# Kernel tuning notes

Measured on AMD Instinct MI355X. Metric: run time of the kernel, lower is better.

Reference implementation:

```python
import jax, jax.numpy as jnp
import numpy as np

B, S, D = 4, 2048, 1024

def setup_inputs() -> dict:
    key = jax.random.key(0)
    ks = jax.random.split(key, 7)
    sc = 1.0 / np.sqrt(D)
    return {
        "x": jax.random.normal(ks[0], (B, S, D), dtype=jnp.float32),
        "Wq": jax.random.normal(ks[1], (D, D), dtype=jnp.float32) * sc,
        "bq": jax.random.normal(ks[2], (D,), dtype=jnp.float32) * 0.01,
        "Wk": jax.random.normal(ks[3], (D, D), dtype=jnp.float32) * sc,
        "bk": jax.random.normal(ks[4], (D,), dtype=jnp.float32) * 0.01,
        "Wv": jax.random.normal(ks[5], (D, D), dtype=jnp.float32) * sc,
        "bv": jax.random.normal(ks[6], (D,), dtype=jnp.float32) * 0.01,
    }

def reference(x, Wq, bq, Wk, bk, Wv, bv):
    # q, k, v: [B, S, D] projections (torch Linear: x @ W^T + b; here W stored as [in, out])
    q = jnp.einsum("bsd,df->bsf", x, Wq) + bq
    k = jnp.einsum("bsd,df->bsf", x, Wk) + bk
    v = jnp.einsum("bsd,df->bsf", x, Wv) + bv
    dim = x.shape[-1]
    # scores: [B, S, S], scaled by sqrt(full d_model) as in the source
    scores = jnp.einsum("bqd,bkd->bqk", q, k) / jnp.sqrt(jnp.float32(dim)).astype(x.dtype)
    attn = jax.nn.softmax(scores, axis=-1)
    return jnp.einsum("bqk,bkd->bqd", attn, v)
```

## Files before the change

### kernel.cpp

```cpp
#include <hip/hip_runtime.h>
#include <hip/hip_bf16.h>

typedef __attribute__((ext_vector_type(8))) short bf16x8;
typedef __attribute__((ext_vector_type(4))) float f32x4;
typedef unsigned short u16;

__device__ __forceinline__ u16 f2bf(float f) {
  unsigned int u = __builtin_bit_cast(unsigned int, f);
  u += 0x7fffu + ((u >> 16) & 1u);
  return (u16)(u >> 16);
}
__device__ __forceinline__ float bf2f(unsigned int h) {
  unsigned int u = h << 16;
  return __builtin_bit_cast(float, u);
}

__device__ __forceinline__ void gload_lds16(const void* g, void* l) {
  __builtin_amdgcn_global_load_lds(
      (const __attribute__((address_space(1))) void*)g,
      (__attribute__((address_space(3))) void*)l, 16, 0, 0);
}

#define BAR() __builtin_amdgcn_s_barrier()
#define LGKM0() asm volatile("s_waitcnt lgkmcnt(0)" ::: "memory")
#define LGKM8() asm volatile("s_waitcnt lgkmcnt(8)" ::: "memory")
#define VMC(N) asm volatile("s_waitcnt vmcnt(%0)" ::"n"(N) : "memory")

template <int EPI>
__global__ __launch_bounds__(512, 2) void gemm8x(
    const u16* __restrict__ Abase, const u16* __restrict__ Btbase,
    const float* __restrict__ bq, const float* __restrict__ bk,
    const float* __restrict__ bv, void* __restrict__ out0,
    void* __restrict__ out1, void* __restrict__ out2, int Kd, int ldc,
    long long sAz, long long sBz, long long sCz) {
  constexpr int HSZ = 16384;
  constexpr int BUFSZ = 4 * HSZ;
  __shared__ char lds[2 * BUFSZ];

  const int tid = threadIdx.x;
  const int w = tid >> 6, l = tid & 63;
  const int wr = w >> 2, wc = w & 3;
  const int lq = l >> 4, lr = l & 15;
  const int bm = blockIdx.y * 256, bn = blockIdx.x * 256;
  const int z = blockIdx.z;
  const u16* A = Abase + (size_t)z * sAz;
  const u16* Bt = Btbase + (size_t)z * sBz;
  const int NTk = Kd >> 6, NI = NTk >> 1;

  const int kbp = ((tid & 7) ^ ((tid >> 3) & 7)) * 8;
  const int drow = tid >> 3;
  const u16* gA[2][2];
  const u16* gB[2][2];
#pragma unroll
  for (int h = 0; h < 2; ++h)
#pragma unroll
    for (int u = 0; u < 2; ++u) {
      gA[h][u] = A + (size_t)(bm + h * 128 + u * 64 + drow) * Kd + kbp;
      gB[h][u] = Bt + (size_t)(bn + h * 128 + u * 64 + drow) * Kd + kbp;
    }

  auto stageA = [&](int buf, int h, int kt) {
    char* d = lds + buf * BUFSZ + h * HSZ + tid * 16;
    gload_lds16(gA[h][0] + kt * 64, d);
    gload_lds16(gA[h][1] + kt * 64, d + 8192);
  };
  auto stageB = [&](int buf, int h, int kt) {
    char* d = lds + buf * BUFSZ + (2 + h) * HSZ + tid * 16;
    gload_lds16(gB[h][0] + kt * 64, d);
    gload_lds16(gB[h][1] + kt * 64, d + 8192);
  };

  const int rA = wr * 64 + lr;
  const int rB = wc * 32 + lr;
  int aoff[2], boff[2];
#pragma unroll
  for (int kh = 0; kh < 2; ++kh) {
    aoff[kh] = rA * 128 + (((kh * 4 + lq) ^ (rA & 7)) << 4);
    boff[kh] = rB * 128 + (((kh * 4 + lq) ^ (rB & 7)) << 4);
  }

  f32x4 acc[2][4][2][2] = {};
  bf16x8 a[2][4];
  bf16x8 bb[2][2][2];

#define RD_A(BUF, MQ)                                                       \
  {                                                                         \
    const char* p_ = lds + (BUF)*BUFSZ + (MQ)*HSZ;                          \
    _Pragma("unroll") for (int kh = 0; kh < 2; ++kh)                        \
        _Pragma("unroll") for (int mf = 0; mf < 4; ++mf) a[kh][mf] =        \
            *(const bf16x8*)(p_ + aoff[kh] + mf * 2048);                    \
  }
#define RD_B(BUF, NQ)                                                       \
  {                                                                         \
    const char* p_ = lds + (BUF)*BUFSZ + (2 + (NQ)) * HSZ;                  \
    _Pragma("unroll") for (int kh = 0; kh < 2; ++kh)                        \
        _Pragma("unroll") for (int nf = 0; nf < 2; ++nf) bb[NQ][kh][nf] =   \
            *(const bf16x8*)(p_ + boff[kh] + nf * 2048);                    \
  }
#define MMAQ(MQ, NQ)                                                          \
  {                                                                           \
    __builtin_amdgcn_s_setprio(1);                                            \
    _Pragma("unroll") for (int kh = 0; kh < 2; ++kh)                          \
        _Pragma("unroll") for (int mf = 0; mf < 4; ++mf)                      \
            _Pragma("unroll") for (int nf = 0; nf < 2; ++nf) acc[MQ][mf][NQ]  \
                [nf] = __builtin_amdgcn_mfma_f32_16x16x32_bf16(               \
                    a[kh][mf], bb[NQ][kh][nf], acc[MQ][mf][NQ][nf], 0, 0, 0); \
    __builtin_amdgcn_s_setprio(0);                                            \
  }

  stageA(0, 0, 0);
  stageB(0, 0, 0);
  stageB(0, 1, 0);
  stageA(0, 1, 0);
  stageA(1, 0, 1);
  stageB(1, 0, 1);
  stageB(1, 1, 1);
  VMC(6);
  BAR();

  for (int i = 0; i < NI; ++i) {
    const int kt1 = 2 * i + 1, ktn0 = 2 * i + 2, ktn1 = 2 * i + 3;
    const bool s0 = ktn0 < NTk, s1 = ktn1 < NTk;
    RD_A(0, 0);
    RD_B(0, 0);
    stageA(1, 1, kt1);
    LGKM8();
    BAR();
    LGKM0();
    MMAQ(0, 0);
    BAR();
    RD_B(0, 1);
    if (s0) stageA(0, 0, ktn0);
    BAR();
    LGKM0();
    MMAQ(0, 1);
    BAR();
    RD_A(0, 1);
    if (s0) stageB(0, 0, ktn0);
    BAR();
    LGKM0();
    MMAQ(1, 1);
    BAR();
    if (s0) stageB(0, 1, ktn0);
    BAR();
    MMAQ(1, 0);
    if (i + 1 < NI) VMC(6); else VMC(0);
    BAR();
    RD_A(1, 0);
    RD_B(1, 0);
    if (s0) stageA(0, 1, ktn0);
    LGKM8();
    BAR();
    LGKM0();
    MMAQ(0, 0);
    BAR();
    RD_B(1, 1);
    if (s1) stageA(1, 0, ktn1);
    BAR();
    LGKM0();
    MMAQ(0, 1);
    BAR();
    RD_A(1, 1);
    if (s1) stageB(1, 0, ktn1);
    BAR();
    LGKM0();
    MMAQ(1, 1);
    BAR();
    if (s1) stageB(1, 1, ktn1);
    BAR();
    MMAQ(1, 0);
    VMC(6);
    BAR();
  }

  if constexpr (EPI == 0) {
    const int mat = bn >> 10;
    const float sc = (mat == 0) ? 0.03125f : 1.0f;
    const float* bias = (mat == 0) ? bq : (mat == 1 ? bk : bv);
    u16* Q = (u16*)out0;
    u16* K = (u16*)out1;
    u16* V = (u16*)out2;
#pragma unroll
    for (int nq = 0; nq < 2; ++nq)
#pragma unroll
      for (int nf = 0; nf < 2; ++nf) {
        const int oc = ((bn + wc * 32 + nq * 128 + nf * 16 + lr) & 1023);
        const float bv2 = bias[oc];
#pragma unroll
        for (int mq = 0; mq < 2; ++mq)
#pragma unroll
          for (int mf = 0; mf < 4; ++mf) {
            const int row = bm + wr * 64 + mq * 128 + mf * 16 + lq * 4;
            if (mat < 2) {
              u16* dst = (mat == 0) ? Q : K;
#pragma unroll
              for (int e = 0; e < 4; ++e)
                dst[(size_t)(row + e) * 1024 + oc] =
                    f2bf((acc[mq][mf][nq][nf][e] + bv2) * sc);
            } else {
              const int bz = row >> 11, sdx = row & 2047;
              ushort4 pk;
              pk.x = f2bf(acc[mq][mf][nq][nf][0] + bv2);
              pk.y = f2bf(acc[mq][mf][nq][nf][1] + bv2);
              pk.z = f2bf(acc[mq][mf][nq][nf][2] + bv2);
              pk.w = f2bf(acc[mq][mf][nq][nf][3] + bv2);
              *(ushort4*)&V[((size_t)bz * 1024 + oc) * 2048 + sdx] = pk;
            }
          }
      }
  } else {
    u16* C = (u16*)out0 + (size_t)z * sCz;
#pragma unroll
    for (int nq = 0; nq < 2; ++nq)
#pragma unroll
      for (int nf = 0; nf < 2; ++nf) {
        const int col = bn + wc * 32 + nq * 128 + nf * 16 + lr;
#pragma unroll
        for (int mq = 0; mq < 2; ++mq)
#pragma unroll
          for (int mf = 0; mf < 4; ++mf) {
            const int row = bm + wr * 64 + mq * 128 + mf * 16 + lq * 4;
#pragma unroll
            for (int e = 0; e < 4; ++e)
              C[(size_t)(row + e) * ldc + col] = f2bf(acc[mq][mf][nq][nf][e]);
          }
      }
  }
#undef RD_A
#undef RD_B
#undef MMAQ
}

__global__ __launch_bounds__(512, 2) void gemm2v(
    const u16* __restrict__ Abase, const u16* __restrict__ Btbase,
    float* __restrict__ outp, int Kd, int ldc, long long sAz, long long sBz,
    long long sCz) {
  constexpr int ASZ = 16384;
  constexpr int BSZ = 32768;
  constexpr int BBASE = 2 * ASZ;
  __shared__ char lds[2 * ASZ + 3 * BSZ];

  const int tid = threadIdx.x;
  const int w = tid >> 6, l = tid & 63;
  const int wr = w >> 2, wc = w & 3;
  const int lq = l >> 4, lr = l & 15;
  const int bm = blockIdx.y * 128, bn = blockIdx.x * 256;
  const int z = blockIdx.z;
  const u16* A = Abase + (size_t)z * sAz;
  const u16* Bt = Btbase + (size_t)z * sBz;
  const int NT = Kd >> 6;

  const int kbp = ((tid & 7) ^ ((tid >> 3) & 7)) * 8;
  const int drow = tid >> 3;
  const u16* gA[2];
  const u16* gB[4];
#pragma unroll
  for (int u = 0; u < 2; ++u)
    gA[u] = A + (size_t)(bm + u * 64 + drow) * Kd + kbp;
#pragma unroll
  for (int u = 0; u < 4; ++u)
    gB[u] = Bt + (size_t)(bn + u * 64 + drow) * Kd + kbp;

  auto stageA = [&](int kt) {
    char* d = lds + (kt & 1) * ASZ + tid * 16;
#pragma unroll
    for (int u = 0; u < 2; ++u) gload_lds16(gA[u] + kt * 64, d + u * 8192);
  };
  auto stageB = [&](int kt) {
    char* d = lds + BBASE + (kt % 3) * BSZ + tid * 16;
#pragma unroll
    for (int u = 0; u < 4; ++u) gload_lds16(gB[u] + kt * 64, d + u * 8192);
  };

  const int rA = wr * 64 + lr;
  const int rB0 = wc * 64 + lr;
  int aoff[2];
#pragma unroll
  for (int kh = 0; kh < 2; ++kh)
    aoff[kh] = rA * 128 + (((kh * 4 + lq) ^ (rA & 7)) << 4);

  f32x4 acc[4][2][2] = {};
  bf16x8 a[2][4], b[2][2];

  auto rdA = [&](int kt) {
    const char* p = lds + (kt & 1) * ASZ;
#pragma unroll
    for (int kh = 0; kh < 2; ++kh)
#pragma unroll
      for (int mf = 0; mf < 4; ++mf)
        a[kh][mf] = *(const bf16x8*)(p + aoff[kh] + mf * 2048);
  };
  auto rdB = [&](int kt, int nh) {
    const char* p = lds + BBASE + (kt % 3) * BSZ;
    const int rB = rB0 + nh * 32;
#pragma unroll
    for (int kh = 0; kh < 2; ++kh) {
      const int o = rB * 128 + (((kh * 4 + lq) ^ (rB & 7)) << 4);
#pragma unroll
      for (int nf = 0; nf < 2; ++nf)
        b[kh][nf] = *(const bf16x8*)(p + o + nf * 2048);
    }
  };
  auto mma = [&](int nh) {
    __builtin_amdgcn_s_setprio(1);
#pragma unroll
    for (int kh = 0; kh < 2; ++kh)
#pragma unroll
      for (int mf = 0; mf < 4; ++mf)
#pragma unroll
        for (int nf = 0; nf < 2; ++nf)
          acc[mf][nh][nf] = __builtin_amdgcn_mfma_f32_16x16x32_bf16(
              a[kh][mf], b[kh][nf], acc[mf][nh][nf], 0, 0, 0);
    __builtin_amdgcn_s_setprio(0);
  };

  stageB(0);
  stageA(0);
  stageB(1);
  stageA(1);
  VMC(6);
  BAR();

  for (int t = 0; t < NT; ++t) {
    rdA(t);
    rdB(t, 0);
    if (t + 2 < NT) stageB(t + 2);
    LGKM8();
    BAR();
    LGKM0();
    mma(0);
    BAR();
    rdB(t, 1);
    if (t + 2 < NT) stageA(t + 2);
    BAR();
    LGKM0();
    mma(1);
    if (t + 3 <= NT) VMC(6); else VMC(0);
    BAR();
  }

  float* C = outp + (size_t)z * sCz;
#pragma unroll
  for (int nh = 0; nh < 2; ++nh)
#pragma unroll
    for (int nf = 0; nf < 2; ++nf) {
      const int col = bn + wc * 64 + nh * 32 + nf * 16 + lr;
#pragma unroll
      for (int mf = 0; mf < 4; ++mf) {
        const int row = bm + wr * 64 + mf * 16 + lq * 4;
#pragma unroll
        for (int e = 0; e < 4; ++e)
          C[(size_t)(row + e) * ldc + col] = acc[mf][nh][nf][e];
      }
    }
}

__global__ __launch_bounds__(256) void cvt_x(const float* __restrict__ in,
                                             u16* __restrict__ out) {
  const int i = blockIdx.x * 256 + threadIdx.x;
  const float4 v = ((const float4*)in)[i];
  ushort4 o;
  o.x = f2bf(v.x);
  o.y = f2bf(v.y);
  o.z = f2bf(v.z);
  o.w = f2bf(v.w);
  ((ushort4*)out)[i] = o;
}

__global__ void cvt_wt(const float* __restrict__ Wq,
                       const float* __restrict__ Wk,
                       const float* __restrict__ Wv, u16* __restrict__ Wt) {
  __shared__ float s[32][33];
  const float* W = blockIdx.z == 0 ? Wq : (blockIdx.z == 1 ? Wk : Wv);
  u16* O = Wt + (size_t)blockIdx.z * 1048576;
  const int k0 = blockIdx.y * 32, n0 = blockIdx.x * 32;
  s[threadIdx.y][threadIdx.x] =
      W[(size_t)(k0 + threadIdx.y) * 1024 + n0 + threadIdx.x];
  __syncthreads();
  O[(size_t)(n0 + threadIdx.y) * 1024 + k0 + threadIdx.x] =
      f2bf(s[threadIdx.x][threadIdx.y]);
}

__global__ __launch_bounds__(256) void softmax_rows(u16* __restrict__ SP) {
  const size_t base = ((size_t)blockIdx.y * 2048 + blockIdx.x) * 2048;
  u16* p = SP + base;
  const int t = threadIdx.x;
  __shared__ float red[4];

  uint4 u = ((const uint4*)p)[t];
  unsigned int uu[4] = {u.x, u.y, u.z, u.w};
  float f[8];
#pragma unroll
  for (int j = 0; j < 4; ++j) {
    f[2 * j] = bf2f(uu[j] & 0xffffu);
    f[2 * j + 1] = __builtin_bit_cast(float, uu[j] & 0xffff0000u);
  }
  float mx = f[0];
#pragma unroll
  for (int i = 1; i < 8; ++i) mx = fmaxf(mx, f[i]);
#pragma unroll
  for (int o = 32; o; o >>= 1) mx = fmaxf(mx, __shfl_xor(mx, o, 64));
  if ((t & 63) == 0) red[t >> 6] = mx;
  __syncthreads();
  mx = fmaxf(fmaxf(red[0], red[1]), fmaxf(red[2], red[3]));
  __syncthreads();

  float e[8];
  float sum = 0.f;
#pragma unroll
  for (int i = 0; i < 8; ++i) {
    e[i] = __expf(f[i] - mx);
    sum += e[i];
  }
#pragma unroll
  for (int o = 32; o; o >>= 1) sum += __shfl_xor(sum, o, 64);
  if ((t & 63) == 0) red[t >> 6] = sum;
  __syncthreads();
  sum = red[0] + red[1] + red[2] + red[3];
  const float inv = 1.0f / sum;

  uint4 ov;
  unsigned int w0[4];
#pragma unroll
  for (int j = 0; j < 4; ++j) {
    unsigned int lo = f2bf(e[2 * j] * inv);
    unsigned int hi = f2bf(e[2 * j + 1] * inv);
    w0[j] = lo | (hi << 16);
  }
  ov.x = w0[0];
  ov.y = w0[1];
  ov.z = w0[2];
  ov.w = w0[3];
  ((uint4*)p)[t] = ov;
}

extern "C" void kernel_launch(void* const* d_in, const int* in_sizes, int n_in,
                              void* d_out, int out_size, void* d_ws,
                              size_t ws_size, hipStream_t stream) {
  const float* x = (const float*)d_in[0];
  const float* Wq = (const float*)d_in[1];
  const float* bq = (const float*)d_in[2];
  const float* Wk = (const float*)d_in[3];
  const float* bk = (const float*)d_in[4];
  const float* Wv = (const float*)d_in[5];
  const float* bv = (const float*)d_in[6];
  float* out = (float*)d_out;
  char* ws = (char*)d_ws;

  u16* xb = (u16*)ws;
  u16* Wt = (u16*)(ws + 16777216);
  u16* Qb = (u16*)(ws + 23068672);
  u16* Kb = Qb + 8388608;
  u16* Vt = Kb + 8388608;
  u16* SP = Vt + 8388608;

  cvt_x<<<8192, 256, 0, stream>>>(x, xb);
  cvt_wt<<<dim3(32, 32, 3), dim3(32, 32), 0, stream>>>(Wq, Wk, Wv, Wt);

  gemm8x<0><<<dim3(12, 32, 1), 512, 0, stream>>>(
      xb, Wt, bq, bk, bv, Qb, Kb, Vt, 1024, 0, 0, 0, 0);

  gemm8x<2><<<dim3(8, 8, 4), 512, 0, stream>>>(
      Qb, Kb, nullptr, nullptr, nullptr, SP, nullptr, nullptr, 1024, 2048,
      2097152LL, 2097152LL, 4194304LL);

  softmax_rows<<<dim3(2048, 4), 256, 0, stream>>>(SP);

  gemm2v<<<dim3(4, 16, 4), 512, 0, stream>>>(
      SP, Vt, out, 2048, 1024, 4194304LL, 2097152LL, 2097152LL);
}
```

Measured before the change: 181.1 us.

## Restructure GEMM main loops with fewer barriers and split A register sets

Rewrites the software pipelines of both GEMM kernels. The 256x256 kernel now iterates one k-tile per loop step. It keeps separate even and odd A fragment register sets, reads both B quarters up front, and removes explicit lgkmcnt waits and several barriers. The gemm2v kernel reads all B fragments at once, splits the MMA by k-half instead of n-half, and drops a barrier per iteration. The aim is to cut synchronisation overhead and let LDS reads overlap MFMA, at the cost of more register pressure and reliance on compiler-inserted waits for correctness.

```diff
diff --git a/kernel.cpp b/kernel.cpp
--- a/kernel.cpp
+++ b/kernel.cpp
@@ -22,8 +22,6 @@
 }
 
 #define BAR() __builtin_amdgcn_s_barrier()
-#define LGKM0() asm volatile("s_waitcnt lgkmcnt(0)" ::: "memory")
-#define LGKM8() asm volatile("s_waitcnt lgkmcnt(8)" ::: "memory")
 #define VMC(N) asm volatile("s_waitcnt vmcnt(%0)" ::"n"(N) : "memory")
 
 template <int EPI>
@@ -45,7 +43,7 @@
   const int z = blockIdx.z;
   const u16* A = Abase + (size_t)z * sAz;
   const u16* Bt = Btbase + (size_t)z * sBz;
-  const int NTk = Kd >> 6, NI = NTk >> 1;
+  const int NTk = Kd >> 6;
 
   const int kbp = ((tid & 7) ^ ((tid >> 3) & 7)) * 8;
   const int drow = tid >> 3;
@@ -80,31 +78,39 @@
   }
 
   f32x4 acc[2][4][2][2] = {};
-  bf16x8 a[2][4];
+  bf16x8 aE[2][4], aO[2][4];
   bf16x8 bb[2][2][2];
 
-#define RD_A(BUF, MQ)                                                       \
-  {                                                                         \
-    const char* p_ = lds + (BUF)*BUFSZ + (MQ)*HSZ;                          \
-    _Pragma("unroll") for (int kh = 0; kh < 2; ++kh)                        \
-        _Pragma("unroll") for (int mf = 0; mf < 4; ++mf) a[kh][mf] =        \
-            *(const bf16x8*)(p_ + aoff[kh] + mf * 2048);                    \
-  }
-#define RD_B(BUF, NQ)                                                       \
-  {                                                                         \
-    const char* p_ = lds + (BUF)*BUFSZ + (2 + (NQ)) * HSZ;                  \
-    _Pragma("unroll") for (int kh = 0; kh < 2; ++kh)                        \
-        _Pragma("unroll") for (int nf = 0; nf < 2; ++nf) bb[NQ][kh][nf] =   \
-            *(const bf16x8*)(p_ + boff[kh] + nf * 2048);                    \
-  }
-#define MMAQ(MQ, NQ)                                                          \
+#define RD_AE(BUF)                                                        \
+  {                                                                       \
+    const char* p_ = lds + (BUF)*BUFSZ;                                   \
+    _Pragma("unroll") for (int kh = 0; kh < 2; ++kh)                      \
+        _Pragma("unroll") for (int mf = 0; mf < 4; ++mf) aE[kh][mf] =     \
+            *(const bf16x8*)(p_ + aoff[kh] + mf * 2048);                  \
+  }
+#define RD_AO(BUF)                                                        \
+  {                                                                       \
+    const char* p_ = lds + (BUF)*BUFSZ + HSZ;                             \
+    _Pragma("unroll") for (int kh = 0; kh < 2; ++kh)                      \
+        _Pragma("unroll") for (int mf = 0; mf < 4; ++mf) aO[kh][mf] =     \
+            *(const bf16x8*)(p_ + aoff[kh] + mf * 2048);                  \
+  }
+#define RD_B(BUF, NQ)                                                     \
+  {                                                                       \
+    const char* p_ = lds + (BUF)*BUFSZ + (2 + (NQ)) * HSZ;                \
+    _Pragma("unroll") for (int kh = 0; kh < 2; ++kh)                      \
+        _Pragma("unroll") for (int nf = 0; nf < 2; ++nf) bb[NQ][kh][nf] = \
+            *(const bf16x8*)(p_ + boff[kh] + nf * 2048);                  \
+  }
+#define MMAQ(MQ, NQ, ASET)                                                    \
   {                                                                           \
     __builtin_amdgcn_s_setprio(1);                                            \
     _Pragma("unroll") for (int kh = 0; kh < 2; ++kh)                          \
         _Pragma("unroll") for (int mf = 0; mf < 4; ++mf)                      \
             _Pragma("unroll") for (int nf = 0; nf < 2; ++nf) acc[MQ][mf][NQ]  \
                 [nf] = __builtin_amdgcn_mfma_f32_16x16x32_bf16(               \
-                    a[kh][mf], bb[NQ][kh][nf], acc[MQ][mf][NQ][nf], 0, 0, 0); \
+                    ASET[kh][mf], bb[NQ][kh][nf], acc[MQ][mf][NQ][nf], 0, 0,  \
+                    0);                                                       \
     __builtin_amdgcn_s_setprio(0);                                            \
   }
 
@@ -118,59 +124,29 @@
   VMC(6);
   BAR();
 
-  for (int i = 0; i < NI; ++i) {
-    const int kt1 = 2 * i + 1, ktn0 = 2 * i + 2, ktn1 = 2 * i + 3;
-    const bool s0 = ktn0 < NTk, s1 = ktn1 < NTk;
-    RD_A(0, 0);
-    RD_B(0, 0);
-    stageA(1, 1, kt1);
-    LGKM8();
-    BAR();
-    LGKM0();
-    MMAQ(0, 0);
-    BAR();
-    RD_B(0, 1);
-    if (s0) stageA(0, 0, ktn0);
-    BAR();
-    LGKM0();
-    MMAQ(0, 1);
-    BAR();
-    RD_A(0, 1);
-    if (s0) stageB(0, 0, ktn0);
-    BAR();
-    LGKM0();
-    MMAQ(1, 1);
-    BAR();
-    if (s0) stageB(0, 1, ktn0);
-    BAR();
-    MMAQ(1, 0);
-    if (i + 1 < NI) VMC(6); else VMC(0);
-    BAR();
-    RD_A(1, 0);
-    RD_B(1, 0);
-    if (s0) stageA(0, 1, ktn0);
-    LGKM8();
-    BAR();
-    LGKM0();
-    MMAQ(0, 0);
-    BAR();
-    RD_B(1, 1);
-    if (s1) stageA(1, 0, ktn1);
-    BAR();
-    LGKM0();
-    MMAQ(0, 1);
-    BAR();
-    RD_A(1, 1);
-    if (s1) stageB(1, 0, ktn1);
-    BAR();
-    LGKM0();
-    MMAQ(1, 1);
-    BAR();
-    if (s1) stageB(1, 1, ktn1);
-    BAR();
-    MMAQ(1, 0);
-    VMC(6);
-    BAR();
+  for (int t = 0; t < NTk; ++t) {
+    const int buf = t & 1;
+    const bool deep = (t + 2 < NTk);
+    if (deep) VMC(6); else VMC(0);
+    RD_AE(buf);
+    RD_B(buf, 0);
+    RD_B(buf, 1);
+    if (t + 1 < NTk) stageA(buf ^ 1, 1, t + 1);
+    BAR();
+    MMAQ(0, 0, aE);
+    if (deep) VMC(6); else VMC(0);
+    RD_AO(buf);
+    if (deep) stageA(buf, 0, t + 2);
+    BAR();
+    MMAQ(0, 1, aE);
+    if (deep) VMC(6); else VMC(0);
+    if (deep) stageB(buf, 0, t + 2);
+    BAR();
+    MMAQ(1, 1, aO);
+    if (deep) VMC(6); else VMC(0);
+    if (deep) stageB(buf, 1, t + 2);
+    BAR();
+    MMAQ(1, 0, aO);
   }
 
   if constexpr (EPI == 0) {
@@ -226,7 +202,8 @@
           }
       }
   }
-#undef RD_A
+#undef RD_AE
+#undef RD_AO
 #undef RD_B
 #undef MMAQ
 }
@@ -280,7 +257,8 @@
     aoff[kh] = rA * 128 + (((kh * 4 + lq) ^ (rA & 7)) << 4);
 
   f32x4 acc[4][2][2] = {};
-  bf16x8 a[2][4], b[2][2];
+  bf16x8 a[2][4];
+  bf16x8 bb[2][2][2];
 
   auto rdA = [&](int kt) {
     const char* p = lds + (kt & 1) * ASZ;
@@ -290,27 +268,30 @@
       for (int mf = 0; mf < 4; ++mf)
         a[kh][mf] = *(const bf16x8*)(p + aoff[kh] + mf * 2048);
   };
-  auto rdB = [&](int kt, int nh) {
+  auto rdB = [&](int kt) {
     const char* p = lds + BBASE + (kt % 3) * BSZ;
-    const int rB = rB0 + nh * 32;
-#pragma unroll
-    for (int kh = 0; kh < 2; ++kh) {
-      const int o = rB * 128 + (((kh * 4 + lq) ^ (rB & 7)) << 4);
-#pragma unroll
-      for (int nf = 0; nf < 2; ++nf)
-        b[kh][nf] = *(const bf16x8*)(p + o + nf * 2048);
+#pragma unroll
+    for (int nh = 0; nh < 2; ++nh) {
+      const int rB = rB0 + nh * 32;
+#pragma unroll
+      for (int kh = 0; kh < 2; ++kh) {
+        const int o = rB * 128 + (((kh * 4 + lq) ^ (rB & 7)) << 4);
+#pragma unroll
+        for (int nf = 0; nf < 2; ++nf)
+          bb[nh][kh][nf] = *(const bf16x8*)(p + o + nf * 2048);
+      }
     }
   };
-  auto mma = [&](int nh) {
+  auto mma = [&](int kh) {
     __builtin_amdgcn_s_setprio(1);
 #pragma unroll
-    for (int kh = 0; kh < 2; ++kh)
+    for (int nh = 0; nh < 2; ++nh)
 #pragma unroll
       for (int mf = 0; mf < 4; ++mf)
 #pragma unroll
         for (int nf = 0; nf < 2; ++nf)
           acc[mf][nh][nf] = __builtin_amdgcn_mfma_f32_16x16x32_bf16(
-              a[kh][mf], b[kh][nf], acc[mf][nh][nf], 0, 0, 0);
+              a[kh][mf], bb[nh][kh][nf], acc[mf][nh][nf], 0, 0, 0);
     __builtin_amdgcn_s_setprio(0);
   };
 
@@ -323,20 +304,14 @@
 
   for (int t = 0; t < NT; ++t) {
     rdA(t);
-    rdB(t, 0);
+    rdB(t);
     if (t + 2 < NT) stageB(t + 2);
-    LGKM8();
-    BAR();
-    LGKM0();
+    BAR();
     mma(0);
-    BAR();
-    rdB(t, 1);
+    if (t + 2 < NT) VMC(4); else VMC(0);
     if (t + 2 < NT) stageA(t + 2);
     BAR();
-    LGKM0();
     mma(1);
-    if (t + 3 <= NT) VMC(6); else VMC(0);
-    BAR();
   }
 
   float* C = outp + (size_t)z * sCz;
```

New measurement: 177.0 us. -2.2%, faster.
